# Kernel optimization log

Hardware: AMD Instinct MI355X
Metric: run time of the kernel (lower is better)

Reference implementation:

```python
import jax, jax.numpy as jnp
import numpy as np

B, T, C, H = 4, 1024, 1024, 16
HS = C // H  # head_size = 64
EPS = 1e-5


def layer_norm(x, w, b):
    mu = jnp.mean(x, axis=-1, keepdims=True)
    var = jnp.mean(jnp.square(x - mu), axis=-1, keepdims=True)
    return (x - mu) * jax.lax.rsqrt(var + EPS) * w + b


def setup_inputs() -> dict:
    key = jax.random.key(0)
    ks = jax.random.split(key, 12)
    s = 0.02
    return {
        "x": jax.random.normal(ks[0], (B, T, C), jnp.float32),
        "ln1_w": jnp.ones((C,), jnp.float32),
        "ln1_b": jnp.zeros((C,), jnp.float32),
        "Wk": jax.random.normal(ks[1], (H, C, HS), jnp.float32) * s,
        "Wq": jax.random.normal(ks[2], (H, C, HS), jnp.float32) * s,
        "Wv": jax.random.normal(ks[3], (H, C, HS), jnp.float32) * s,
        "Wo": jax.random.normal(ks[4], (C, C), jnp.float32) * s,
        "bo": jnp.zeros((C,), jnp.float32),
        "ln2_w": jnp.ones((C,), jnp.float32),
        "ln2_b": jnp.zeros((C,), jnp.float32),
        "W1": jax.random.normal(ks[5], (C, 4 * C), jnp.float32) * s,
        "b1": jnp.zeros((4 * C,), jnp.float32),
        "prelu_a": jnp.asarray(0.25, jnp.float32),
        "W2": jax.random.normal(ks[6], (4 * C, C), jnp.float32) * s,
        "b2": jnp.zeros((C,), jnp.float32),
    }


def reference(x, ln1_w, ln1_b, Wk, Wq, Wv, Wo, bo, ln2_w, ln2_b, W1, b1, prelu_a, W2, b2):
    # --- self-attention branch (pre-LN) ---
    h = layer_norm(x, ln1_w, ln1_b)  # [B,T,C]
    k = jnp.einsum('btc,hcd->bhtd', h, Wk)
    q = jnp.einsum('btc,hcd->bhtd', h, Wq)
    v = jnp.einsum('btc,hcd->bhtd', h, Wv)
    # NOTE: source computes k @ q^T (not q @ k^T) scaled by n_embd**-0.5
    wei = jnp.einsum('bhtd,bhsd->bhts', k, q) * (C ** -0.5)  # [B,H,T,T]
    causal = jnp.tril(jnp.ones((T, T), bool))
    wei = jnp.where(causal, wei, -jnp.inf)
    wei = jax.nn.softmax(wei, axis=-1)
    out = jnp.einsum('bhts,bhsd->bthd', wei, v).reshape(B, T, C)
    out = out @ Wo + bo
    x = x + out
    # --- feed-forward branch (pre-LN) ---
    h2 = layer_norm(x, ln2_w, ln2_b)
    f = h2 @ W1 + b1
    f = jnp.where(f > 0, f, prelu_a * f)  # PReLU, single scalar param
    f = f @ W2 + b2
    return x + f
```

## Files before the change

kernel.cpp:

```cpp
#include <hip/hip_runtime.h>


typedef __bf16 bf16_t;
typedef __attribute__((ext_vector_type(8))) __bf16 bfx8;
typedef __attribute__((ext_vector_type(4))) __bf16 bfx4;
typedef __attribute__((ext_vector_type(4))) float f32x4;
typedef __attribute__((ext_vector_type(8))) unsigned short u16x8;
typedef unsigned int u32;

#define MFMA_BF16(a, b, c) __builtin_amdgcn_mfma_f32_16x16x32_bf16((a), (b), (c), 0, 0, 0)
#define GLOAD_LDS16(g, l)                                                     \
  __builtin_amdgcn_global_load_lds((__attribute__((address_space(1))) void*)(g), \
                                   (__attribute__((address_space(3))) void*)(l), 16, 0, 0)
#define BARX()                      \
  __builtin_amdgcn_s_barrier();     \
  __builtin_amdgcn_sched_barrier(0)
#define VMW6()                                     \
  asm volatile("s_waitcnt vmcnt(6)" ::: "memory"); \
  __builtin_amdgcn_sched_barrier(0)
#define VMW0()                                     \
  asm volatile("s_waitcnt vmcnt(0)" ::: "memory"); \
  __builtin_amdgcn_sched_barrier(0)

__global__ __launch_bounds__(256) void ln_kernel(const float* __restrict__ x,
                                                 const float* __restrict__ w,
                                                 const float* __restrict__ b,
                                                 bf16_t* __restrict__ out) {
  const int row = blockIdx.x;
  const int tid = threadIdx.x;
  const float4 v = reinterpret_cast<const float4*>(x + (size_t)row * 1024)[tid];
  float s = v.x + v.y + v.z + v.w;
  float s2 = v.x * v.x + v.y * v.y + v.z * v.z + v.w * v.w;
#pragma unroll
  for (int off = 1; off < 64; off <<= 1) {
    s += __shfl_xor(s, off);
    s2 += __shfl_xor(s2, off);
  }
  __shared__ float red[8];
  const int wv = tid >> 6;
  if ((tid & 63) == 0) {
    red[wv] = s;
    red[4 + wv] = s2;
  }
  __syncthreads();
  s = red[0] + red[1] + red[2] + red[3];
  s2 = red[4] + red[5] + red[6] + red[7];
  const float mu = s * (1.0f / 1024.0f);
  const float rs = rsqrtf(s2 * (1.0f / 1024.0f) - mu * mu + 1e-5f);
  const float4 wv4 = reinterpret_cast<const float4*>(w)[tid];
  const float4 bv4 = reinterpret_cast<const float4*>(b)[tid];
  bfx4 o;
  o[0] = (bf16_t)((v.x - mu) * rs * wv4.x + bv4.x);
  o[1] = (bf16_t)((v.y - mu) * rs * wv4.y + bv4.y);
  o[2] = (bf16_t)((v.z - mu) * rs * wv4.z + bv4.z);
  o[3] = (bf16_t)((v.w - mu) * rs * wv4.w + bv4.w);
  reinterpret_cast<bfx4*>(out + (size_t)row * 1024)[tid] = o;
}

__device__ __forceinline__ void tc_body(const float* __restrict__ in,
                                        bf16_t* __restrict__ out, int K, int N, int k0,
                                        int n0, float (*tile)[65], int t) {
  const int rl = t >> 4, cl = (t & 15) * 4;
#pragma unroll
  for (int p = 0; p < 4; ++p) {
    const int r = p * 16 + rl;
    const float4 v = *reinterpret_cast<const float4*>(in + (size_t)(k0 + r) * N + n0 + cl);
    tile[r][cl] = v.x;
    tile[r][cl + 1] = v.y;
    tile[r][cl + 2] = v.z;
    tile[r][cl + 3] = v.w;
  }
  __syncthreads();
#pragma unroll
  for (int p = 0; p < 2; ++p) {
    const int idx = p * 256 + t;
    const int n = idx >> 3, kc = (idx & 7) * 8;
    bfx8 o;
#pragma unroll
    for (int i = 0; i < 8; ++i) o[i] = (bf16_t)tile[kc + i][n];
    *reinterpret_cast<bfx8*>(out + (size_t)(n0 + n) * K + k0 + kc) = o;
  }
}

__global__ __launch_bounds__(256) void transpose_cast(const float* __restrict__ in,
                                                      bf16_t* __restrict__ out, int K,
                                                      int N) {
  __shared__ float tile[64][65];
  tc_body(in, out, K, N, blockIdx.x * 64, blockIdx.y * 64, tile, threadIdx.x);
}

__global__ __launch_bounds__(256) void transpose_qkv(const float* __restrict__ Wq,
                                                     const float* __restrict__ Wk,
                                                     const float* __restrict__ Wv,
                                                     bf16_t* __restrict__ out) {
  __shared__ float tile[64][65];
  const int z = blockIdx.y;
  const int sel = z >> 4, h = z & 15;
  const float* in = ((sel == 0) ? Wq : (sel == 1) ? Wk : Wv) + h * 65536;
  bf16_t* o = out + (size_t)sel * 1048576 + h * 65536;
  tc_body(in, o, 1024, 64, blockIdx.x * 64, 0, tile, threadIdx.x);
}

enum { EPI_QKV = 0, EPI_WO = 1, EPI_MLP1 = 2, EPI_FINAL = 3 };

template <int EPI, int BM, int BN, int NT>
__global__ __launch_bounds__(NT, 2) void gemm_bt(
    const bf16_t* __restrict__ A, const bf16_t* __restrict__ BT,
    const float* __restrict__ bias, const float* __restrict__ res,
    const float* __restrict__ prelu, float* __restrict__ outf,
    bf16_t* __restrict__ ob0, bf16_t* __restrict__ ob1, bf16_t* __restrict__ ob2,
    int K, int N) {
  constexpr int WM = 2;
  constexpr int WN = NT / 64 / WM;
  constexpr int MF = BM / WM / 16;
  constexpr int NF = BN / WN / 16;
  constexpr int ACH = BM * 64 / (NT * 8);
  constexpr int BCH = BN * 64 / (NT * 8);
  constexpr int LOADS = ACH + BCH;
  static_assert(LOADS == 8 || LOADS == 6, "add a vmcnt case");
  __shared__ __align__(16) bf16_t sA[2][BM * 64];
  __shared__ __align__(16) bf16_t sB[2][BN * 64];
  const int tid = threadIdx.x;
  const int lane = tid & 63;
  const int w = tid >> 6;
  const int wr = w / WN, wc = w % WN;
  const int g = lane >> 4, l15 = lane & 15;
  const int row0 = blockIdx.x * BM, col0 = blockIdx.y * BN;
  const int rowbase = row0 + wr * (BM / WM);
  const int colbase = wc * (BN / WN);

  f32x4 acc[MF][NF] = {};

  auto stage = [&](int k0, int buf) {
#pragma unroll
    for (int j = 0; j < ACH; ++j) {
      const int chunk = j * NT + tid;
      const int r = chunk >> 3, c = chunk & 7;
      GLOAD_LDS16(A + (size_t)(row0 + r) * K + k0 + ((c ^ (r & 7)) * 8),
                  sA[buf] + chunk * 8);
    }
#pragma unroll
    for (int j = 0; j < BCH; ++j) {
      const int chunk = j * NT + tid;
      const int r = chunk >> 3, c = chunk & 7;
      GLOAD_LDS16(BT + (size_t)(col0 + r) * K + k0 + ((c ^ (r & 7)) * 8),
                  sB[buf] + chunk * 8);
    }
  };

  stage(0, 0);
  const int nk = K >> 6;
  for (int t = 0; t < nk; ++t) {
    const int cur = t & 1;
    if (t + 1 < nk) {
      stage((t + 1) << 6, cur ^ 1);
      __builtin_amdgcn_sched_barrier(0);
      if constexpr (LOADS == 8)
        asm volatile("s_waitcnt vmcnt(8)" ::: "memory");
      else
        asm volatile("s_waitcnt vmcnt(6)" ::: "memory");
    } else {
      __builtin_amdgcn_sched_barrier(0);
      asm volatile("s_waitcnt vmcnt(0)" ::: "memory");
    }
    __builtin_amdgcn_s_barrier();
    __builtin_amdgcn_sched_barrier(0);
    const bf16_t* __restrict__ pA = sA[cur];
    const bf16_t* __restrict__ pB = sB[cur];
#pragma unroll
    for (int kk = 0; kk < 2; ++kk) {
      bfx8 af[MF], bfr[NF];
#pragma unroll
      for (int m = 0; m < MF; ++m) {
        const int r = wr * (BM / WM) + m * 16 + l15;
        const int c = (kk * 4 + g) ^ (r & 7);
        af[m] = *reinterpret_cast<const bfx8*>(pA + r * 64 + c * 8);
      }
#pragma unroll
      for (int n = 0; n < NF; ++n) {
        const int r = colbase + n * 16 + l15;
        const int c = (kk * 4 + g) ^ (r & 7);
        bfr[n] = *reinterpret_cast<const bfx8*>(pB + r * 64 + c * 8);
      }
#pragma unroll
      for (int m = 0; m < MF; ++m)
#pragma unroll
        for (int n = 0; n < NF; ++n) acc[m][n] = MFMA_BF16(af[m], bfr[n], acc[m][n]);
    }
    __builtin_amdgcn_sched_barrier(0);
    __builtin_amdgcn_s_barrier();
  }

  const float pa = (EPI == EPI_MLP1) ? prelu[0] : 0.0f;
#pragma unroll
  for (int m = 0; m < MF; ++m) {
#pragma unroll
    for (int n = 0; n < NF; ++n) {
#pragma unroll
      for (int j = 0; j < 4; ++j) {
        const int row = rowbase + m * 16 + (g << 2) + j;
        const int col = col0 + colbase + n * 16 + l15;
        const float v = acc[m][n][j];
        if (EPI == EPI_QKV) {
          const int sel = col >> 10;
          const int h = (col >> 6) & 15, d = col & 63;
          const int bb = row >> 10, t = row & 1023;
          bf16_t* dst = (sel == 0) ? ob0 : (sel == 1) ? ob1 : ob2;
          dst[((size_t)(bb * 16 + h) * 1024 + t) * 64 + d] = (bf16_t)v;
        } else if (EPI == EPI_MLP1) {
          float t = v + bias[col];
          t = (t > 0.0f) ? t : pa * t;
          ob0[(size_t)row * N + col] = (bf16_t)t;
        } else {
          outf[(size_t)row * N + col] = v + bias[col] + res[(size_t)row * N + col];
        }
      }
    }
  }
}

__device__ __forceinline__ void stageA8(const bf16_t* __restrict__ A, int K, int row0,
                                        int k0, int mh, bf16_t* dst, int tid) {
#pragma unroll
  for (int g2 = 0; g2 < 2; ++g2) {
    const int band = g2 * 128 + mh * 64;
    const int row = band + (tid >> 3);
    GLOAD_LDS16(A + (size_t)(row0 + row) * K + k0 + (((tid & 7) ^ (row & 7)) * 8),
                dst + band * 64 + tid * 8);
  }
}

__device__ __forceinline__ void stageB8(const bf16_t* __restrict__ BT, int K, int col0,
                                        int k0, int nh, bf16_t* dst, int tid) {
#pragma unroll
  for (int g2 = 0; g2 < 2; ++g2) {
    const int rho = g2 * 64 + (tid >> 3);
    const int grow = (rho >> 5) * 64 + nh * 32 + (rho & 31);
    GLOAD_LDS16(BT + (size_t)(col0 + grow) * K + k0 + (((tid & 7) ^ (rho & 7)) * 8),
                dst + nh * 8192 + g2 * 4096 + tid * 8);
  }
}

template <int MH, int NH, bool LOADA>
__device__ __forceinline__ void quad8(const bf16_t* __restrict__ pA,
                                      const bf16_t* __restrict__ pB, int wr, int wc,
                                      int l15, int g, bfx8 (&af)[4][2],
                                      f32x4 (&acc)[8][4]) {
  if (LOADA) {
#pragma unroll
    for (int i = 0; i < 4; ++i) {
      const int r = wr * 128 + (MH * 4 + i) * 16 + l15;
#pragma unroll
      for (int kk = 0; kk < 2; ++kk)
        af[i][kk] =
            *reinterpret_cast<const bfx8*>(pA + r * 64 + (((kk * 4 + g) ^ (r & 7)) * 8));
    }
  }
  bfx8 bfr[2][2];
#pragma unroll
  for (int i = 0; i < 2; ++i) {
    const int rho = wc * 32 + i * 16 + l15;
#pragma unroll
    for (int kk = 0; kk < 2; ++kk)
      bfr[i][kk] = *reinterpret_cast<const bfx8*>(pB + NH * 8192 + rho * 64 +
                                                  (((kk * 4 + g) ^ (rho & 7)) * 8));
  }
  __builtin_amdgcn_s_setprio(1);
#pragma unroll
  for (int i = 0; i < 4; ++i)
#pragma unroll
    for (int jn = 0; jn < 2; ++jn)
#pragma unroll
      for (int kk = 0; kk < 2; ++kk)
        acc[MH * 4 + i][NH * 2 + jn] =
            MFMA_BF16(af[i][kk], bfr[jn][kk], acc[MH * 4 + i][NH * 2 + jn]);
  __builtin_amdgcn_s_setprio(0);
}

__global__ __launch_bounds__(512, 2) void gemm_8ph_mlp1(
    const bf16_t* __restrict__ A, const bf16_t* __restrict__ BT,
    const float* __restrict__ bias, const float* __restrict__ prelu,
    bf16_t* __restrict__ outb, int K, int N) {
  __shared__ __align__(16) bf16_t sA[2][256 * 64];
  __shared__ __align__(16) bf16_t sB[2][256 * 64];
  const int tid = threadIdx.x;
  const int lane = tid & 63;
  const int w = tid >> 6;
  const int wr = w >> 2, wc = w & 3;
  const int g = lane >> 4, l15 = lane & 15;
  const int row0 = blockIdx.x * 256, col0 = blockIdx.y * 256;

  f32x4 acc[8][4] = {};
  bfx8 af[4][2];

  stageA8(A, K, row0, 0, 0, sA[0], tid);
  stageB8(BT, K, col0, 0, 0, sB[0], tid);
  stageB8(BT, K, col0, 0, 1, sB[0], tid);
  stageA8(A, K, row0, 0, 1, sA[0], tid);
  stageA8(A, K, row0, 64, 0, sA[1], tid);
  stageB8(BT, K, col0, 64, 0, sB[1], tid);

  const int nt = K >> 7;
  for (int j = 0; j < nt; ++j) {
    const bool more = (j + 1 < nt);
    const int ku1 = (2 * j + 1) << 6, k2 = (2 * j + 2) << 6, k3 = (2 * j + 3) << 6;
    BARX();
    stageB8(BT, K, col0, ku1, 1, sB[1], tid);
    VMW6();
    BARX();
    quad8<0, 0, true>(sA[0], sB[0], wr, wc, l15, g, af, acc);
    BARX();
    stageA8(A, K, row0, ku1, 1, sA[1], tid);
    quad8<0, 1, false>(sA[0], sB[0], wr, wc, l15, g, af, acc);
    BARX();
    if (more) stageA8(A, K, row0, k2, 0, sA[0], tid);
    quad8<1, 0, true>(sA[0], sB[0], wr, wc, l15, g, af, acc);
    BARX();
    if (more) stageB8(BT, K, col0, k2, 0, sB[0], tid);
    quad8<1, 1, false>(sA[0], sB[0], wr, wc, l15, g, af, acc);
    BARX();
    if (more) {
      stageB8(BT, K, col0, k2, 1, sB[0], tid);
      VMW6();
    } else {
      VMW0();
    }
    BARX();
    quad8<0, 0, true>(sA[1], sB[1], wr, wc, l15, g, af, acc);
    BARX();
    if (more) stageA8(A, K, row0, k2, 1, sA[0], tid);
    quad8<0, 1, false>(sA[1], sB[1], wr, wc, l15, g, af, acc);
    BARX();
    if (more) stageA8(A, K, row0, k3, 0, sA[1], tid);
    quad8<1, 0, true>(sA[1], sB[1], wr, wc, l15, g, af, acc);
    BARX();
    if (more) stageB8(BT, K, col0, k3, 0, sB[1], tid);
    quad8<1, 1, false>(sA[1], sB[1], wr, wc, l15, g, af, acc);
  }

  const float pa = prelu[0];
#pragma unroll
  for (int m = 0; m < 8; ++m) {
#pragma unroll
    for (int n = 0; n < 4; ++n) {
#pragma unroll
      for (int j = 0; j < 4; ++j) {
        const int row = row0 + wr * 128 + m * 16 + (g << 2) + j;
        const int col = col0 + wc * 64 + n * 16 + l15;
        float t = acc[m][n][j] + bias[col];
        t = (t > 0.0f) ? t : pa * t;
        outb[(size_t)row * N + col] = (bf16_t)t;
      }
    }
  }
}

__global__ __launch_bounds__(256) void attn_kernel(const bf16_t* __restrict__ kproj,
                                                   const bf16_t* __restrict__ qproj,
                                                   const bf16_t* __restrict__ vproj,
                                                   bf16_t* __restrict__ att) {
  __shared__ __align__(16) bf16_t sK[2][64 * 64];
  __shared__ __align__(16) bf16_t sVt[2][64 * 64];
  __shared__ __align__(16) bf16_t sP[4][16 * 64];
  const int tid = threadIdx.x, lane = tid & 63, w = tid >> 6;
  const int g = lane >> 4, l15 = lane & 15;
  const int bh = blockIdx.y;
  const size_t head = (size_t)bh * (1024 * 64);
  const int b = bh >> 4, h = bh & 15;
  const int vrow = 2 * (tid >> 3);
  const int vdb = tid & 7;

  for (int half = 0; half < 2; ++half) {
    const int tb = half ? (15 - (int)blockIdx.x) : (int)blockIdx.x;
    const int t0 = tb * 64;
    const int nsb = tb + 1;

    __syncthreads();

    bfx8 aq0, aq1;
    {
      const bf16_t* qrow = kproj + head + (size_t)(t0 + w * 16 + l15) * 64 + g * 8;
      aq0 = *reinterpret_cast<const bfx8*>(qrow);
      aq1 = *reinterpret_cast<const bfx8*>(qrow + 32);
    }

    {
#pragma unroll
      for (int j = 0; j < 2; ++j) {
        const int chunk = j * 256 + tid;
        const int r = chunk >> 3, c = chunk & 7;
        const int cs = c ^ (r & 7);
        GLOAD_LDS16(qproj + head + (size_t)r * 64 + cs * 8, sK[0] + chunk * 8);
      }
      const bf16_t* vp = vproj + head + (size_t)vrow * 64 + vdb * 8;
      const u16x8 v0 = *reinterpret_cast<const u16x8*>(vp);
      const u16x8 v1 = *reinterpret_cast<const u16x8*>(vp + 64);
#pragma unroll
      for (int i = 0; i < 8; ++i) {
        const int d = vdb * 8 + i;
        const int cc = ((vrow >> 3) ^ i ^ vdb) & 7;
        const u32 pk = ((u32)v1[i] << 16) | (u32)v0[i];
        *reinterpret_cast<u32*>(sVt[0] + d * 64 + cc * 8 + (vrow & 7)) = pk;
      }
    }
    __syncthreads();

    f32x4 accO[4] = {};
    float mrun[4], lrun[4];
#pragma unroll
    for (int j = 0; j < 4; ++j) {
      mrun[j] = -1e30f;
      lrun[j] = 0.0f;
    }

    for (int sb = 0; sb < nsb; ++sb) {
      const int cur = sb & 1;
      const bool pf = (sb + 1 < nsb);
      u16x8 v0n, v1n;
      if (pf) {
        const int s0n = (sb + 1) * 64;
#pragma unroll
        for (int j = 0; j < 2; ++j) {
          const int chunk = j * 256 + tid;
          const int r = chunk >> 3, c = chunk & 7;
          const int cs = c ^ (r & 7);
          GLOAD_LDS16(qproj + head + (size_t)(s0n + r) * 64 + cs * 8, sK[cur ^ 1] + chunk * 8);
        }
        const bf16_t* vp = vproj + head + (size_t)(s0n + vrow) * 64 + vdb * 8;
        v0n = *reinterpret_cast<const u16x8*>(vp);
        v1n = *reinterpret_cast<const u16x8*>(vp + 64);
      }

      f32x4 accS[4] = {};
      const bf16_t* sKc = sK[cur];
#pragma unroll
      for (int kk = 0; kk < 2; ++kk) {
        const bfx8 aq = kk ? aq1 : aq0;
#pragma unroll
        for (int n = 0; n < 4; ++n) {
          const int r = n * 16 + l15;
          const int c = (kk * 4 + g) ^ (r & 7);
          const bfx8 bk = *reinterpret_cast<const bfx8*>(sKc + r * 64 + c * 8);
          accS[n] = MFMA_BF16(aq, bk, accS[n]);
        }
      }

      const int rbase = t0 + w * 16 + (g << 2);
      const int cbase = sb * 64 + l15;
#pragma unroll
      for (int j = 0; j < 4; ++j) {
        const int t = rbase + j;
        float mx = -1e30f;
#pragma unroll
        for (int n = 0; n < 4; ++n) {
          float v = accS[n][j] * 0.03125f;
          v = ((cbase + n * 16) <= t) ? v : -1e30f;
          accS[n][j] = v;
          mx = fmaxf(mx, v);
        }
        mx = fmaxf(mx, __shfl_xor(mx, 1));
        mx = fmaxf(mx, __shfl_xor(mx, 2));
        mx = fmaxf(mx, __shfl_xor(mx, 4));
        mx = fmaxf(mx, __shfl_xor(mx, 8));
        const float mnew = fmaxf(mrun[j], mx);
        const float al = __expf(mrun[j] - mnew);
        float rsum = 0.0f;
#pragma unroll
        for (int n = 0; n < 4; ++n) {
          const float p = __expf(accS[n][j] - mnew);
          accS[n][j] = p;
          rsum += p;
        }
        rsum += __shfl_xor(rsum, 1);
        rsum += __shfl_xor(rsum, 2);
        rsum += __shfl_xor(rsum, 4);
        rsum += __shfl_xor(rsum, 8);
        lrun[j] = lrun[j] * al + rsum;
        mrun[j] = mnew;
#pragma unroll
        for (int n = 0; n < 4; ++n) accO[n][j] *= al;
      }

      bf16_t* sPw = sP[w];
#pragma unroll
      for (int n = 0; n < 4; ++n)
#pragma unroll
        for (int j = 0; j < 4; ++j) {
          const int r = (g << 2) + j;
          const int s = n * 16 + l15;
          const int cc = (s >> 3) ^ (r & 7);
          sPw[r * 64 + cc * 8 + (s & 7)] = (bf16_t)accS[n][j];
        }

      const bf16_t* sVc = sVt[cur];
#pragma unroll
      for (int kk = 0; kk < 2; ++kk) {
        bfx8 ap;
        {
          const int r = l15;
          const int c = (kk * 4 + g) ^ (r & 7);
          ap = *reinterpret_cast<const bfx8*>(sPw + r * 64 + c * 8);
        }
#pragma unroll
        for (int n = 0; n < 4; ++n) {
          const int d = n * 16 + l15;
          const int c = (kk * 4 + g) ^ (d & 7) ^ ((d >> 3) & 7);
          const bfx8 bv = *reinterpret_cast<const bfx8*>(sVc + d * 64 + c * 8);
          accO[n] = MFMA_BF16(ap, bv, accO[n]);
        }
      }

      if (pf) {
#pragma unroll
        for (int i = 0; i < 8; ++i) {
          const int d = vdb * 8 + i;
          const int cc = ((vrow >> 3) ^ i ^ vdb) & 7;
          const u32 pk = ((u32)v1n[i] << 16) | (u32)v0n[i];
          *reinterpret_cast<u32*>(sVt[cur ^ 1] + d * 64 + cc * 8 + (vrow & 7)) = pk;
        }
      }
      __syncthreads();
    }

#pragma unroll
    for (int j = 0; j < 4; ++j) {
      const float inv = 1.0f / lrun[j];
      const int t = t0 + w * 16 + (g << 2) + j;
#pragma unroll
      for (int n = 0; n < 4; ++n) {
        const int d = n * 16 + l15;
        att[((size_t)(b * 1024 + t)) * 1024 + h * 64 + d] = (bf16_t)(accO[n][j] * inv);
      }
    }
  }
}

extern "C" void kernel_launch(void* const* d_in, const int* in_sizes, int n_in,
                              void* d_out, int out_size, void* d_ws, size_t ws_size,
                              hipStream_t stream) {
  (void)in_sizes; (void)n_in; (void)out_size; (void)ws_size;
  const float* x = (const float*)d_in[0];
  const float* ln1w = (const float*)d_in[1];
  const float* ln1b = (const float*)d_in[2];
  const float* Wk = (const float*)d_in[3];
  const float* Wq = (const float*)d_in[4];
  const float* Wv = (const float*)d_in[5];
  const float* Wo = (const float*)d_in[6];
  const float* bo = (const float*)d_in[7];
  const float* ln2w = (const float*)d_in[8];
  const float* ln2b = (const float*)d_in[9];
  const float* W1 = (const float*)d_in[10];
  const float* b1 = (const float*)d_in[11];
  const float* pa = (const float*)d_in[12];
  const float* W2 = (const float*)d_in[13];
  const float* b2 = (const float*)d_in[14];
  float* out = (float*)d_out;
  char* ws = (char*)d_ws;
  const size_t MB = 1ull << 20;
  bf16_t* h1 = (bf16_t*)(ws + 0 * MB);
  bf16_t* h2 = (bf16_t*)(ws + 8 * MB);
  bf16_t* qb = (bf16_t*)(ws + 16 * MB);
  bf16_t* kb = (bf16_t*)(ws + 24 * MB);
  bf16_t* vb = (bf16_t*)(ws + 32 * MB);
  bf16_t* attb = (bf16_t*)(ws + 40 * MB);
  bf16_t* fbuf = (bf16_t*)(ws + 48 * MB);
  bf16_t* WqkvT = (bf16_t*)(ws + 80 * MB);
  bf16_t* WoT = (bf16_t*)(ws + 86 * MB);
  bf16_t* W1T = (bf16_t*)(ws + 88 * MB);
  bf16_t* W2T = (bf16_t*)(ws + 96 * MB);

  transpose_qkv<<<dim3(16, 48), 256, 0, stream>>>(Wq, Wk, Wv, WqkvT);
  transpose_cast<<<dim3(16, 16), 256, 0, stream>>>(Wo, WoT, 1024, 1024);
  transpose_cast<<<dim3(16, 64), 256, 0, stream>>>(W1, W1T, 1024, 4096);
  transpose_cast<<<dim3(64, 16), 256, 0, stream>>>(W2, W2T, 4096, 1024);

  ln_kernel<<<4096, 256, 0, stream>>>(x, ln1w, ln1b, h1);
  gemm_bt<EPI_QKV, 256, 256, 512><<<dim3(16, 12), 512, 0, stream>>>(
      h1, WqkvT, nullptr, nullptr, nullptr, nullptr, qb, kb, vb, 1024, 3072);
  attn_kernel<<<dim3(8, 64), 256, 0, stream>>>(kb, qb, vb, attb);
  gemm_bt<EPI_WO, 64, 128, 256><<<dim3(64, 8), 256, 0, stream>>>(
      attb, WoT, bo, x, nullptr, out, nullptr, nullptr, nullptr, 1024, 1024);
  ln_kernel<<<4096, 256, 0, stream>>>(out, ln2w, ln2b, h2);
  gemm_8ph_mlp1<<<dim3(16, 16), 512, 0, stream>>>(h2, W1T, b1, pa, fbuf, 1024, 4096);
  gemm_bt<EPI_FINAL, 64, 128, 256><<<dim3(64, 8), 256, 0, stream>>>(
      fbuf, W2T, b2, out, nullptr, out, nullptr, nullptr, nullptr, 4096, 1024);
}
```

Baseline: 225.3 us.

## Split-K the MLP2 GEMM with the 8-phase kernel plus reduction; skip causal mask off-diagonal

```diff
diff --git a/kernel.cpp b/kernel.cpp
--- a/kernel.cpp
+++ b/kernel.cpp
@@ -101,15 +101,14 @@
   tc_body(in, o, 1024, 64, blockIdx.x * 64, 0, tile, threadIdx.x);
 }
 
-enum { EPI_QKV = 0, EPI_WO = 1, EPI_MLP1 = 2, EPI_FINAL = 3 };
+enum { EPI_QKV = 0, EPI_WO = 1 };
 
 template <int EPI, int BM, int BN, int NT>
 __global__ __launch_bounds__(NT, 2) void gemm_bt(
     const bf16_t* __restrict__ A, const bf16_t* __restrict__ BT,
     const float* __restrict__ bias, const float* __restrict__ res,
-    const float* __restrict__ prelu, float* __restrict__ outf,
-    bf16_t* __restrict__ ob0, bf16_t* __restrict__ ob1, bf16_t* __restrict__ ob2,
-    int K, int N) {
+    float* __restrict__ outf, bf16_t* __restrict__ ob0, bf16_t* __restrict__ ob1,
+    bf16_t* __restrict__ ob2, int K, int N) {
   constexpr int WM = 2;
   constexpr int WN = NT / 64 / WM;
   constexpr int MF = BM / WM / 16;
@@ -191,7 +190,6 @@
     __builtin_amdgcn_s_barrier();
   }
 
-  const float pa = (EPI == EPI_MLP1) ? prelu[0] : 0.0f;
 #pragma unroll
   for (int m = 0; m < MF; ++m) {
 #pragma unroll
@@ -207,10 +205,6 @@
           const int bb = row >> 10, t = row & 1023;
           bf16_t* dst = (sel == 0) ? ob0 : (sel == 1) ? ob1 : ob2;
           dst[((size_t)(bb * 16 + h) * 1024 + t) * 64 + d] = (bf16_t)v;
-        } else if (EPI == EPI_MLP1) {
-          float t = v + bias[col];
-          t = (t > 0.0f) ? t : pa * t;
-          ob0[(size_t)row * N + col] = (bf16_t)t;
         } else {
           outf[(size_t)row * N + col] = v + bias[col] + res[(size_t)row * N + col];
         }
@@ -219,24 +213,24 @@
   }
 }
 
-__device__ __forceinline__ void stageA8(const bf16_t* __restrict__ A, int K, int row0,
+__device__ __forceinline__ void stageA8(const bf16_t* __restrict__ A, int Ks, int row0,
                                         int k0, int mh, bf16_t* dst, int tid) {
 #pragma unroll
   for (int g2 = 0; g2 < 2; ++g2) {
     const int band = g2 * 128 + mh * 64;
     const int row = band + (tid >> 3);
-    GLOAD_LDS16(A + (size_t)(row0 + row) * K + k0 + (((tid & 7) ^ (row & 7)) * 8),
+    GLOAD_LDS16(A + (size_t)(row0 + row) * Ks + k0 + (((tid & 7) ^ (row & 7)) * 8),
                 dst + band * 64 + tid * 8);
   }
 }
 
-__device__ __forceinline__ void stageB8(const bf16_t* __restrict__ BT, int K, int col0,
+__device__ __forceinline__ void stageB8(const bf16_t* __restrict__ BT, int Ks, int col0,
                                         int k0, int nh, bf16_t* dst, int tid) {
 #pragma unroll
   for (int g2 = 0; g2 < 2; ++g2) {
     const int rho = g2 * 64 + (tid >> 3);
     const int grow = (rho >> 5) * 64 + nh * 32 + (rho & 31);
-    GLOAD_LDS16(BT + (size_t)(col0 + grow) * K + k0 + (((tid & 7) ^ (rho & 7)) * 8),
+    GLOAD_LDS16(BT + (size_t)(col0 + grow) * Ks + k0 + (((tid & 7) ^ (rho & 7)) * 8),
                 dst + nh * 8192 + g2 * 4096 + tid * 8);
   }
 }
@@ -277,10 +271,11 @@
   __builtin_amdgcn_s_setprio(0);
 }
 
-__global__ __launch_bounds__(512, 2) void gemm_8ph_mlp1(
+template <bool PRELU>
+__global__ __launch_bounds__(512, 2) void gemm_8ph(
     const bf16_t* __restrict__ A, const bf16_t* __restrict__ BT,
     const float* __restrict__ bias, const float* __restrict__ prelu,
-    bf16_t* __restrict__ outb, int K, int N) {
+    bf16_t* __restrict__ outb, int Ks, int Klen, int N, size_t zstride) {
   __shared__ __align__(16) bf16_t sA[2][256 * 64];
   __shared__ __align__(16) bf16_t sB[2][256 * 64];
   const int tid = threadIdx.x;
@@ -289,38 +284,40 @@
   const int wr = w >> 2, wc = w & 3;
   const int g = lane >> 4, l15 = lane & 15;
   const int row0 = blockIdx.x * 256, col0 = blockIdx.y * 256;
+  const int koff = blockIdx.z * Klen;
 
   f32x4 acc[8][4] = {};
   bfx8 af[4][2];
 
-  stageA8(A, K, row0, 0, 0, sA[0], tid);
-  stageB8(BT, K, col0, 0, 0, sB[0], tid);
-  stageB8(BT, K, col0, 0, 1, sB[0], tid);
-  stageA8(A, K, row0, 0, 1, sA[0], tid);
-  stageA8(A, K, row0, 64, 0, sA[1], tid);
-  stageB8(BT, K, col0, 64, 0, sB[1], tid);
-
-  const int nt = K >> 7;
+  stageA8(A, Ks, row0, koff, 0, sA[0], tid);
+  stageB8(BT, Ks, col0, koff, 0, sB[0], tid);
+  stageB8(BT, Ks, col0, koff, 1, sB[0], tid);
+  stageA8(A, Ks, row0, koff, 1, sA[0], tid);
+  stageA8(A, Ks, row0, koff + 64, 0, sA[1], tid);
+  stageB8(BT, Ks, col0, koff + 64, 0, sB[1], tid);
+
+  const int nt = Klen >> 7;
   for (int j = 0; j < nt; ++j) {
     const bool more = (j + 1 < nt);
-    const int ku1 = (2 * j + 1) << 6, k2 = (2 * j + 2) << 6, k3 = (2 * j + 3) << 6;
-    BARX();
-    stageB8(BT, K, col0, ku1, 1, sB[1], tid);
+    const int ku1 = koff + ((2 * j + 1) << 6), k2 = koff + ((2 * j + 2) << 6),
+              k3 = koff + ((2 * j + 3) << 6);
+    BARX();
+    stageB8(BT, Ks, col0, ku1, 1, sB[1], tid);
     VMW6();
     BARX();
     quad8<0, 0, true>(sA[0], sB[0], wr, wc, l15, g, af, acc);
     BARX();
-    stageA8(A, K, row0, ku1, 1, sA[1], tid);
+    stageA8(A, Ks, row0, ku1, 1, sA[1], tid);
     quad8<0, 1, false>(sA[0], sB[0], wr, wc, l15, g, af, acc);
     BARX();
-    if (more) stageA8(A, K, row0, k2, 0, sA[0], tid);
+    if (more) stageA8(A, Ks, row0, k2, 0, sA[0], tid);
     quad8<1, 0, true>(sA[0], sB[0], wr, wc, l15, g, af, acc);
     BARX();
-    if (more) stageB8(BT, K, col0, k2, 0, sB[0], tid);
+    if (more) stageB8(BT, Ks, col0, k2, 0, sB[0], tid);
     quad8<1, 1, false>(sA[0], sB[0], wr, wc, l15, g, af, acc);
     BARX();
     if (more) {
-      stageB8(BT, K, col0, k2, 1, sB[0], tid);
+      stageB8(BT, Ks, col0, k2, 1, sB[0], tid);
       VMW6();
     } else {
       VMW0();
@@ -328,17 +325,18 @@
     BARX();
     quad8<0, 0, true>(sA[1], sB[1], wr, wc, l15, g, af, acc);
     BARX();
-    if (more) stageA8(A, K, row0, k2, 1, sA[0], tid);
+    if (more) stageA8(A, Ks, row0, k2, 1, sA[0], tid);
     quad8<0, 1, false>(sA[1], sB[1], wr, wc, l15, g, af, acc);
     BARX();
-    if (more) stageA8(A, K, row0, k3, 0, sA[1], tid);
+    if (more) stageA8(A, Ks, row0, k3, 0, sA[1], tid);
     quad8<1, 0, true>(sA[1], sB[1], wr, wc, l15, g, af, acc);
     BARX();
-    if (more) stageB8(BT, K, col0, k3, 0, sB[1], tid);
+    if (more) stageB8(BT, Ks, col0, k3, 0, sB[1], tid);
     quad8<1, 1, false>(sA[1], sB[1], wr, wc, l15, g, af, acc);
   }
 
-  const float pa = prelu[0];
+  bf16_t* o = outb + (size_t)blockIdx.z * zstride;
+  const float pa = PRELU ? prelu[0] : 0.0f;
 #pragma unroll
   for (int m = 0; m < 8; ++m) {
 #pragma unroll
@@ -347,12 +345,40 @@
       for (int j = 0; j < 4; ++j) {
         const int row = row0 + wr * 128 + m * 16 + (g << 2) + j;
         const int col = col0 + wc * 64 + n * 16 + l15;
-        float t = acc[m][n][j] + bias[col];
-        t = (t > 0.0f) ? t : pa * t;
-        outb[(size_t)row * N + col] = (bf16_t)t;
-      }
-    }
-  }
+        float t = acc[m][n][j];
+        if (PRELU) {
+          t += bias[col];
+          t = (t > 0.0f) ? t : pa * t;
+        }
+        o[(size_t)row * N + col] = (bf16_t)t;
+      }
+    }
+  }
+}
+
+__global__ __launch_bounds__(256) void reduce_mlp2(const bf16_t* __restrict__ part,
+                                                   const float* __restrict__ b2,
+                                                   float* __restrict__ out) {
+  const int idx = (blockIdx.x * 256 + threadIdx.x) * 8;
+  const int col = idx & 1023;
+  float a[8];
+  {
+    const float4 o0 = *reinterpret_cast<const float4*>(out + idx);
+    const float4 o1 = *reinterpret_cast<const float4*>(out + idx + 4);
+    const float4 b0 = *reinterpret_cast<const float4*>(b2 + col);
+    const float4 b1 = *reinterpret_cast<const float4*>(b2 + col + 4);
+    a[0] = o0.x + b0.x; a[1] = o0.y + b0.y; a[2] = o0.z + b0.z; a[3] = o0.w + b0.w;
+    a[4] = o1.x + b1.x; a[5] = o1.y + b1.y; a[6] = o1.z + b1.z; a[7] = o1.w + b1.w;
+  }
+#pragma unroll
+  for (int s = 0; s < 4; ++s) {
+    const u16x8 p = *reinterpret_cast<const u16x8*>(part + (size_t)s * 4194304 + idx);
+#pragma unroll
+    for (int i = 0; i < 8; ++i) a[i] += __uint_as_float((u32)p[i] << 16);
+  }
+  float4 r0{a[0], a[1], a[2], a[3]}, r1{a[4], a[5], a[6], a[7]};
+  *reinterpret_cast<float4*>(out + idx) = r0;
+  *reinterpret_cast<float4*>(out + idx + 4) = r1;
 }
 
 __global__ __launch_bounds__(256) void attn_kernel(const bf16_t* __restrict__ kproj,
@@ -416,6 +442,7 @@
     for (int sb = 0; sb < nsb; ++sb) {
       const int cur = sb & 1;
       const bool pf = (sb + 1 < nsb);
+      const bool diag = (sb == tb);
       u16x8 v0n, v1n;
       if (pf) {
         const int s0n = (sb + 1) * 64;
@@ -451,12 +478,21 @@
       for (int j = 0; j < 4; ++j) {
         const int t = rbase + j;
         float mx = -1e30f;
-#pragma unroll
-        for (int n = 0; n < 4; ++n) {
-          float v = accS[n][j] * 0.03125f;
-          v = ((cbase + n * 16) <= t) ? v : -1e30f;
-          accS[n][j] = v;
-          mx = fmaxf(mx, v);
+        if (diag) {
+#pragma unroll
+          for (int n = 0; n < 4; ++n) {
+            float v = accS[n][j] * 0.03125f;
+            v = ((cbase + n * 16) <= t) ? v : -1e30f;
+            accS[n][j] = v;
+            mx = fmaxf(mx, v);
+          }
+        } else {
+#pragma unroll
+          for (int n = 0; n < 4; ++n) {
+            const float v = accS[n][j] * 0.03125f;
+            accS[n][j] = v;
+            mx = fmaxf(mx, v);
+          }
         }
         mx = fmaxf(mx, __shfl_xor(mx, 1));
         mx = fmaxf(mx, __shfl_xor(mx, 2));
@@ -564,6 +600,7 @@
   bf16_t* vb = (bf16_t*)(ws + 32 * MB);
   bf16_t* attb = (bf16_t*)(ws + 40 * MB);
   bf16_t* fbuf = (bf16_t*)(ws + 48 * MB);
+  bf16_t* part = (bf16_t*)(ws + 16 * MB);
   bf16_t* WqkvT = (bf16_t*)(ws + 80 * MB);
   bf16_t* WoT = (bf16_t*)(ws + 86 * MB);
   bf16_t* W1T = (bf16_t*)(ws + 88 * MB);
@@ -576,12 +613,14 @@
 
   ln_kernel<<<4096, 256, 0, stream>>>(x, ln1w, ln1b, h1);
   gemm_bt<EPI_QKV, 256, 256, 512><<<dim3(16, 12), 512, 0, stream>>>(
-      h1, WqkvT, nullptr, nullptr, nullptr, nullptr, qb, kb, vb, 1024, 3072);
+      h1, WqkvT, nullptr, nullptr, nullptr, qb, kb, vb, 1024, 3072);
   attn_kernel<<<dim3(8, 64), 256, 0, stream>>>(kb, qb, vb, attb);
   gemm_bt<EPI_WO, 64, 128, 256><<<dim3(64, 8), 256, 0, stream>>>(
-      attb, WoT, bo, x, nullptr, out, nullptr, nullptr, nullptr, 1024, 1024);
+      attb, WoT, bo, x, out, nullptr, nullptr, nullptr, 1024, 1024);
   ln_kernel<<<4096, 256, 0, stream>>>(out, ln2w, ln2b, h2);
-  gemm_8ph_mlp1<<<dim3(16, 16), 512, 0, stream>>>(h2, W1T, b1, pa, fbuf, 1024, 4096);
-  gemm_bt<EPI_FINAL, 64, 128, 256><<<dim3(64, 8), 256, 0, stream>>>(
-      fbuf, W2T, b2, out, nullptr, out, nullptr, nullptr, nullptr, 4096, 1024);
-}
+  gemm_8ph<true><<<dim3(16, 16, 1), 512, 0, stream>>>(h2, W1T, b1, pa, fbuf, 1024, 1024,
+                                                      4096, 0);
+  gemm_8ph<false><<<dim3(16, 4, 4), 512, 0, stream>>>(fbuf, W2T, nullptr, nullptr, part,
+                                                      4096, 1024, 1024, 4194304);
+  reduce_mlp2<<<2048, 256, 0, stream>>>(part, b2, out);
+}
```

Result: faster. 219.1 us (-2.7%).
